# Kernel tuning notes

Hardware: AMD Instinct MI355X
Metric: run time of the kernel (lower is better)

## Reference

```python
import jax, jax.numpy as jnp
import numpy as np

HEADS = 56
OUT = 32       # hidden_channels (per-head out dim)
N_FEAT = 128
N_CLASS = 2
N_NODES = 20000
N_EDGES = 100000
N_GRAPHS = 50
EPS_BN = 1e-5


def _gat_conv(x, W, att_src, att_dst, bias, src, dst, n, concat):
    # x: [n, in]; W: [in, H*O]; att_*: [H, O]
    h = (x @ W).reshape(n, HEADS, OUT)                     # [n, H, O]
    a_s = jnp.sum(h * att_src, axis=-1)                    # [n, H]
    a_d = jnp.sum(h * att_dst, axis=-1)                    # [n, H]
    e = jax.nn.leaky_relu(a_s[src] + a_d[dst], 0.2)        # [E, H]
    m = jax.ops.segment_max(e, dst, num_segments=n)        # per-dst max
    ex = jnp.exp(e - m[dst])
    den = jax.ops.segment_sum(ex, dst, num_segments=n)
    alpha = ex / den[dst]                                  # segment softmax over incoming edges
    msg = h[src] * alpha[:, :, None]                       # [E, H, O]
    out = jax.ops.segment_sum(msg, dst, num_segments=n)    # [n, H, O]
    if concat:
        return out.reshape(n, HEADS * OUT) + bias
    return out.mean(axis=1) + bias


def _bn_eval(x, gamma, beta, mean, var):
    return (x - mean) * jax.lax.rsqrt(var + EPS_BN) * gamma + beta


def setup_inputs() -> dict:
    key = jax.random.key(0)
    ks = jax.random.split(key, 20)
    d1 = HEADS * OUT
    inp = {
        'x': jax.random.normal(ks[0], (N_NODES, N_FEAT), jnp.float32),
        'edge_index': jax.random.randint(ks[1], (2, N_EDGES), 0, N_NODES, jnp.int32),
        'batch': jnp.sort(jax.random.randint(ks[2], (N_NODES,), 0, N_GRAPHS, jnp.int32)),
        'W1': jax.random.normal(ks[3], (N_FEAT, d1), jnp.float32) * (1.0 / np.sqrt(N_FEAT)),
        'att_src1': jax.random.normal(ks[4], (HEADS, OUT), jnp.float32) * 0.1,
        'att_dst1': jax.random.normal(ks[5], (HEADS, OUT), jnp.float32) * 0.1,
        'b1': jnp.zeros((d1,), jnp.float32),
        'bn1_g': jnp.ones((d1,), jnp.float32),
        'bn1_b': jnp.zeros((d1,), jnp.float32),
        'bn1_m': jax.random.normal(ks[6], (d1,), jnp.float32) * 0.1,
        'bn1_v': jax.random.uniform(ks[7], (d1,), jnp.float32) + 0.5,
        'W2': jax.random.normal(ks[8], (d1, d1), jnp.float32) * (1.0 / np.sqrt(d1)),
        'att_src2': jax.random.normal(ks[9], (HEADS, OUT), jnp.float32) * 0.1,
        'att_dst2': jax.random.normal(ks[10], (HEADS, OUT), jnp.float32) * 0.1,
        'b2': jnp.zeros((OUT,), jnp.float32),
        'bn2_g': jnp.ones((OUT,), jnp.float32),
        'bn2_b': jnp.zeros((OUT,), jnp.float32),
        'bn2_m': jax.random.normal(ks[11], (OUT,), jnp.float32) * 0.1,
        'bn2_v': jax.random.uniform(ks[12], (OUT,), jnp.float32) + 0.5,
        'lin_w': jax.random.normal(ks[13], (OUT, N_CLASS), jnp.float32) * (1.0 / np.sqrt(OUT)),
        'lin_b': jnp.zeros((N_CLASS,), jnp.float32),
    }
    return inp


def reference(x, edge_index, batch, W1, att_src1, att_dst1, b1, bn1_g, bn1_b, bn1_m, bn1_v,
              W2, att_src2, att_dst2, b2, bn2_g, bn2_b, bn2_m, bn2_v, lin_w, lin_b):
    n = x.shape[0]
    loop = jnp.arange(n, dtype=edge_index.dtype)
    src = jnp.concatenate([edge_index[0], loop])   # PyG GATConv add_self_loops=True
    dst = jnp.concatenate([edge_index[1], loop])

    h = jax.nn.elu(_gat_conv(x, W1, att_src1, att_dst1, b1, src, dst, n, concat=True))
    h = _bn_eval(h, bn1_g, bn1_b, bn1_m, bn1_v)
    # dropout p=0.5 is identity in eval
    h = _gat_conv(h, W2, att_src2, att_dst2, b2, src, dst, n, concat=False)
    h = _bn_eval(h, bn2_g, bn2_b, bn2_m, bn2_v)

    sums = jax.ops.segment_sum(h, batch, num_segments=N_GRAPHS)
    cnt = jax.ops.segment_sum(jnp.ones((n, 1), h.dtype), batch, num_segments=N_GRAPHS)
    pooled = sums / jnp.maximum(cnt, 1.0)          # global_mean_pool
    return pooled @ lin_w + lin_b
```

## Files before the change

### kernel.cpp

```cpp
#include <hip/hip_runtime.h>
#include <hip/hip_bf16.h>
#include <hip/hip_fp8.h>
#include <cstdint>
#include <cstddef>

#define NN     20000
#define NF     128
#define NH     56
#define OC     32
#define DD1    1792
#define NE     100000
#define ETOT   120000
#define NG     50
#define EPS_BN 1e-5f
#define GRP    16
#define EB     16

typedef __bf16 bf16x8 __attribute__((ext_vector_type(8)));
typedef float  floatx4 __attribute__((ext_vector_type(4)));
typedef float  floatx2 __attribute__((ext_vector_type(2)));
typedef unsigned int u32;
typedef __attribute__((address_space(1))) u32 gu32;
typedef __attribute__((address_space(3))) u32 lu32;

__device__ __forceinline__ void async_copy16(void* lds, const void* g) {
    __builtin_amdgcn_global_load_lds((gu32*)const_cast<void*>(g), (lu32*)lds, 16, 0, 0);
}

__device__ __forceinline__ void dec_fp8x4(u32 u, float* v) {
#if __has_builtin(__builtin_amdgcn_cvt_pk_f32_fp8)
    floatx2 lo = __builtin_amdgcn_cvt_pk_f32_fp8(u, false);
    floatx2 hi = __builtin_amdgcn_cvt_pk_f32_fp8(u, true);
    v[0] = lo[0]; v[1] = lo[1]; v[2] = hi[0]; v[3] = hi[1];
#else
    #pragma unroll
    for (int b = 0; b < 4; ++b) {
        __hip_fp8_e4m3 t;
        t.__x = (u >> (8 * b)) & 0xff;
        v[b] = (float)t;
    }
#endif
}

__device__ __forceinline__ void fma_fp8x4(u32 u, float a, float* acc) {
    float v[4];
    dec_fp8x4(u, v);
    #pragma unroll
    for (int b = 0; b < 4; ++b) acc[b] += a * v[b];
}

__global__ __launch_bounds__(256) void cast_bf16_kernel(const float* __restrict__ in,
                                                        __hip_bfloat16* __restrict__ out, int n) {
    int i = blockIdx.x * 256 + threadIdx.x;
    if (i < n) out[i] = __float2bfloat16(in[i]);
}

__global__ __launch_bounds__(256) void transpose_cast_kernel(const float* __restrict__ in,
                                                             __hip_bfloat16* __restrict__ out,
                                                             int R, int C) {
    __shared__ float tile[32][33];
    int c0 = blockIdx.x * 32, r0 = blockIdx.y * 32;
    int tx = threadIdx.x & 31, ty = threadIdx.x >> 5;
    #pragma unroll
    for (int i = 0; i < 32; i += 8) {
        int r = r0 + ty + i, c = c0 + tx;
        if (r < R && c < C) tile[ty + i][tx] = in[(size_t)r * C + c];
    }
    __syncthreads();
    #pragma unroll
    for (int i = 0; i < 32; i += 8) {
        int c = c0 + ty + i, r = r0 + tx;
        if (c < C && r < R) out[(size_t)c * R + r] = __float2bfloat16(tile[tx][ty + i]);
    }
}

__global__ __launch_bounds__(256) void hist_kernel(const int* __restrict__ ei, int* __restrict__ deg) {
    int i = blockIdx.x * 256 + threadIdx.x;
    if (i >= ETOT) return;
    int dst = (i < NE) ? ei[NE + i] : (i - NE);
    atomicAdd(&deg[dst], 1);
}

__global__ __launch_bounds__(1024) void scan_kernel(const int* __restrict__ deg,
                                                    int* __restrict__ rowptr,
                                                    int* __restrict__ cursor) {
    __shared__ int buf[1024];
    int t = threadIdx.x;
    const int CH = (NN + 1023) >> 10;
    int base = t * CH;
    int s = 0;
    for (int j = 0; j < CH; ++j) { int idx = base + j; if (idx < NN) s += deg[idx]; }
    buf[t] = s;
    __syncthreads();
    for (int off = 1; off < 1024; off <<= 1) {
        int v = (t >= off) ? buf[t - off] : 0;
        __syncthreads();
        buf[t] += v;
        __syncthreads();
    }
    int run = buf[t] - s;
    for (int j = 0; j < CH; ++j) {
        int idx = base + j;
        if (idx < NN) { rowptr[idx] = run; cursor[idx] = run; run += deg[idx]; }
    }
    if (t == 1023) rowptr[NN] = buf[1023];
}

__global__ __launch_bounds__(256) void scatter_kernel(const int* __restrict__ ei,
                                                      int* __restrict__ cursor,
                                                      int* __restrict__ csr_src) {
    int i = blockIdx.x * 256 + threadIdx.x;
    if (i >= ETOT) return;
    int s, d;
    if (i < NE) { s = ei[i]; d = ei[NE + i]; } else { s = i - NE; d = i - NE; }
    int pos = atomicAdd(&cursor[d], 1);
    csr_src[pos] = s;
}

__global__ __launch_bounds__(512, 2) void gemm_192(const __hip_bfloat16* __restrict__ A,
                                                   const __hip_bfloat16* __restrict__ Bt,
                                                   unsigned char* __restrict__ C8,
                                                   int M, int N, int K) {
    __shared__ __align__(16) unsigned short lds[2][28672];
    const int tid  = threadIdx.x;
    const int lane = tid & 63, wave = tid >> 6;
    const int wm = wave >> 2, wn = wave & 3;

    const int nbx = N >> 8;
    const int nby = (M + 191) / 192;
    const int nwg = nbx * nby;
    const int q = nwg >> 3, r = nwg & 7;
    const int xcd = blockIdx.x & 7, bidx = blockIdx.x >> 3;
    const int wg = (xcd < r ? xcd * (q + 1) : r * (q + 1) + (xcd - r) * q) + bidx;
    const int by = wg / nbx, bx = wg - by * nbx;
    const int m0 = by * 192, n0 = bx << 8;

    const int NT = K >> 6;

    const int qq = lane >> 4, rr = lane & 15;

    auto stageA = [&](int kt, int b) {
        #pragma unroll
        for (int i = 0; i < 3; ++i) {
            int slot = i * 512 + tid;
            int row = slot >> 3, pch = slot & 7;
            int lc = pch ^ (row & 7);
            int gr = m0 + row; if (gr > M - 1) gr = M - 1;
            async_copy16(&lds[b][slot * 8], A + (size_t)gr * K + (kt << 6) + lc * 8);
        }
    };
    auto stageB = [&](int kt, int b) {
        #pragma unroll
        for (int i = 0; i < 4; ++i) {
            int slot = i * 512 + tid;
            int row = slot >> 3, pch = slot & 7;
            int lc = pch ^ (row & 7);
            async_copy16(&lds[b][12288 + slot * 8], Bt + (size_t)(n0 + row) * K + (kt << 6) + lc * 8);
        }
    };

    floatx4 zero = {0.f, 0.f, 0.f, 0.f};
    floatx4 acc[6][4];
    #pragma unroll
    for (int i = 0; i < 6; ++i)
        #pragma unroll
        for (int jj = 0; jj < 4; ++jj) acc[i][jj] = zero;

    bf16x8 aF[3][2], bA[2][2], bB[2][2];

    auto loadA = [&](int b, int mg) {
        #pragma unroll
        for (int mf = 0; mf < 3; ++mf)
            #pragma unroll
            for (int s = 0; s < 2; ++s) {
                int row = wm * 96 + mg * 48 + mf * 16 + rr;
                int pch = (s * 4 + qq) ^ (row & 7);
                aF[mf][s] = *(const bf16x8*)&lds[b][row * 64 + pch * 8];
            }
    };
    auto loadB = [&](int b, bf16x8 (&bF)[2][2], int ng) {
        #pragma unroll
        for (int nf = 0; nf < 2; ++nf)
            #pragma unroll
            for (int s = 0; s < 2; ++s) {
                int row = wn * 64 + (ng * 2 + nf) * 16 + rr;
                int pch = (s * 4 + qq) ^ (row & 7);
                bF[nf][s] = *(const bf16x8*)&lds[b][12288 + row * 64 + pch * 8];
            }
    };
    auto mfmaQ = [&](int mg, int ng, bf16x8 (&bF)[2][2]) {
        #pragma unroll
        for (int mf = 0; mf < 3; ++mf)
            #pragma unroll
            for (int nf = 0; nf < 2; ++nf)
                #pragma unroll
                for (int s = 0; s < 2; ++s)
                    acc[mg * 3 + mf][ng * 2 + nf] = __builtin_amdgcn_mfma_f32_16x16x32_bf16(
                        aF[mf][s], bF[nf][s], acc[mg * 3 + mf][ng * 2 + nf], 0, 0, 0);
    };

#define SB0 __builtin_amdgcn_sched_barrier(0)
#define GBAR do { SB0; __builtin_amdgcn_s_barrier(); SB0; } while (0)

    stageB(0, 0); stageA(0, 0);
    stageB(1, 1); stageA(1, 1);
    SB0;
    asm volatile("s_waitcnt vmcnt(7)" ::: "memory");
    GBAR;

    for (int t = 0; t < NT; ++t) {
        const int p = t & 1;
        int tp = t + 2; while (tp >= NT) tp -= 2;

        loadA(p, 0); loadB(p, bA, 0);
        GBAR;
        __builtin_amdgcn_s_setprio(1);
        mfmaQ(0, 0, bA);
        __builtin_amdgcn_s_setprio(0);
        GBAR;

        loadB(p, bB, 1);
        stageB(tp, p);
        GBAR;
        __builtin_amdgcn_s_setprio(1);
        mfmaQ(0, 1, bB);
        __builtin_amdgcn_s_setprio(0);
        GBAR;

        loadA(p, 1);
        stageA(tp, p);
        SB0;
        asm volatile("s_waitcnt vmcnt(7)" ::: "memory");
        GBAR;
        __builtin_amdgcn_s_setprio(1);
        mfmaQ(1, 1, bB);
        mfmaQ(1, 0, bA);
        __builtin_amdgcn_s_setprio(0);
        GBAR;
    }
#undef GBAR
#undef SB0

    #pragma unroll
    for (int mt = 0; mt < 6; ++mt) {
        #pragma unroll
        for (int r4 = 0; r4 < 4; ++r4) {
            int rowc = m0 + wm * 96 + mt * 16 + (lane >> 4) * 4 + r4;
            if (rowc < M) {
                float v0 = acc[mt][0][r4], v1 = acc[mt][1][r4];
                float v2 = acc[mt][2][r4], v3 = acc[mt][3][r4];
                unsigned char q8[4];
#if __has_builtin(__builtin_amdgcn_cvt_pk_fp8_f32)
                u32 p01 = (u32)__builtin_amdgcn_cvt_pk_fp8_f32(v0, v1, 0, false);
                u32 p23 = (u32)__builtin_amdgcn_cvt_pk_fp8_f32(v2, v3, 0, false);
                q8[0] = p01 & 0xff; q8[1] = (p01 >> 8) & 0xff;
                q8[2] = p23 & 0xff; q8[3] = (p23 >> 8) & 0xff;
#else
                { __hip_fp8_e4m3 t0(v0), t1(v1), t2(v2), t3(v3);
                  q8[0] = t0.__x; q8[1] = t1.__x; q8[2] = t2.__x; q8[3] = t3.__x; }
#endif
                #pragma unroll
                for (int nt = 0; nt < 4; ++nt) {
                    int col = n0 + wn * 64 + nt * 16 + (lane & 15);
                    C8[(size_t)rowc * N + col] = q8[nt];
                }
            }
        }
    }
}

__global__ __launch_bounds__(256) void attn_score(const unsigned char* __restrict__ h8,
                                                  const float* __restrict__ att_src,
                                                  const float* __restrict__ att_dst,
                                                  float* __restrict__ as_,
                                                  float* __restrict__ ad_) {
    int wave = threadIdx.x >> 6, lane = threadIdx.x & 63;
    int node = blockIdx.x * 4 + wave;
    if (node >= NN || lane >= NH) return;
    const uint2* hp = (const uint2*)(h8 + (size_t)node * DD1 + lane * OC);
    float s = 0.f, d = 0.f;
    #pragma unroll
    for (int jj = 0; jj < 4; ++jj) {
        uint2 u2 = hp[jj];
        u32 us[2] = {u2.x, u2.y};
        #pragma unroll
        for (int w = 0; w < 2; ++w) {
            float v[4];
            dec_fp8x4(us[w], v);
            #pragma unroll
            for (int b = 0; b < 4; ++b) {
                int o = jj * 8 + w * 4 + b;
                s += v[b] * att_src[lane * OC + o];
                d += v[b] * att_dst[lane * OC + o];
            }
        }
    }
    as_[(size_t)node * NH + lane] = s;
    ad_[(size_t)node * NH + lane] = d;
}

template <int LAYER>
__device__ __forceinline__ void flush_node(float* acc, float den, int cur, int f, int lane,
                                           const float* __restrict__ bias,
                                           const float* __restrict__ bng,
                                           const float* __restrict__ bnb,
                                           const float* __restrict__ bnm,
                                           const float* __restrict__ bnv,
                                           void* __restrict__ outp) {
    float inv = 1.f / den;
    #pragma unroll
    for (int k = 0; k < 4; ++k) acc[k] *= inv;

    if constexpr (LAYER == 1) {
        int d0 = f * 256 + lane * 4;
        u32 r01, r23;
        {
            float v0 = acc[0] + bias[d0 + 0];
            float v1 = acc[1] + bias[d0 + 1];
            float v2 = acc[2] + bias[d0 + 2];
            float v3 = acc[3] + bias[d0 + 3];
            v0 = v0 > 0.f ? v0 : expm1f(v0);
            v1 = v1 > 0.f ? v1 : expm1f(v1);
            v2 = v2 > 0.f ? v2 : expm1f(v2);
            v3 = v3 > 0.f ? v3 : expm1f(v3);
            v0 = (v0 - bnm[d0 + 0]) * rsqrtf(bnv[d0 + 0] + EPS_BN) * bng[d0 + 0] + bnb[d0 + 0];
            v1 = (v1 - bnm[d0 + 1]) * rsqrtf(bnv[d0 + 1] + EPS_BN) * bng[d0 + 1] + bnb[d0 + 1];
            v2 = (v2 - bnm[d0 + 2]) * rsqrtf(bnv[d0 + 2] + EPS_BN) * bng[d0 + 2] + bnb[d0 + 2];
            v3 = (v3 - bnm[d0 + 3]) * rsqrtf(bnv[d0 + 3] + EPS_BN) * bng[d0 + 3] + bnb[d0 + 3];
            __hip_bfloat16 b0 = __float2bfloat16(v0), b1 = __float2bfloat16(v1);
            __hip_bfloat16 b2 = __float2bfloat16(v2), b3 = __float2bfloat16(v3);
            r01 = (u32)*(unsigned short*)&b0 | ((u32)*(unsigned short*)&b1 << 16);
            r23 = (u32)*(unsigned short*)&b2 | ((u32)*(unsigned short*)&b3 << 16);
        }
        uint2 pk; pk.x = r01; pk.y = r23;
        *(uint2*)((__hip_bfloat16*)outp + (size_t)cur * DD1 + d0) = pk;
    } else {
        #pragma unroll
        for (int k = 0; k < 4; ++k) {
            acc[k] += __shfl_xor(acc[k], 8, 64);
            acc[k] += __shfl_xor(acc[k], 16, 64);
            acc[k] += __shfl_xor(acc[k], 32, 64);
        }
        if (lane < 8) {
            floatx4 pk;
            #pragma unroll
            for (int k = 0; k < 4; ++k) pk[k] = acc[k] * (1.f / NH);
            *(floatx4*)((float*)outp + ((size_t)cur * 7 + f) * OC + lane * 4) = pk;
        }
    }
    acc[0] = acc[1] = acc[2] = acc[3] = 0.f;
}

template <int LAYER>
__global__ __launch_bounds__(256) void attn_aggregate(const int* __restrict__ rowptr,
                                                      const int* __restrict__ csr_src,
                                                      const float* __restrict__ as_,
                                                      const float* __restrict__ ad_,
                                                      const unsigned char* __restrict__ h8,
                                                      const float* __restrict__ bias,
                                                      const float* __restrict__ bng,
                                                      const float* __restrict__ bnb,
                                                      const float* __restrict__ bnm,
                                                      const float* __restrict__ bnv,
                                                      void* __restrict__ outp) {
    const int wv = threadIdx.x >> 6, lane = threadIdx.x & 63;
    const int w = blockIdx.x * 4 + wv;
    const int NWAVES = 7 * (NN / GRP);
    if (w >= NWAVES) return;
    const int f  = w % 7;
    const int g  = w / 7;
    const int n0 = g * GRP;
    const int off  = f * 256 + lane * 4;
    const int head = f * 8 + (lane >> 3);

    const int e0 = rowptr[n0], e1 = rowptr[n0 + GRP];
    int cur = n0;
    int bound = rowptr[n0 + 1];
    float adv = ad_[(size_t)cur * NH + head];

    float acc[4] = {0.f, 0.f, 0.f, 0.f};
    float m = -1e30f, den = 0.f;

    for (int e = e0; e < e1; e += EB) {
        u32   hv[EB];
        float sv[EB];
        #pragma unroll
        for (int i = 0; i < EB; ++i) {
            int idx = (e + i < e1) ? e + i : e1 - 1;
            int s = csr_src[idx];
            hv[i] = *(const u32*)(h8 + (size_t)s * DD1 + off);
            sv[i] = as_[(size_t)s * NH + head];
        }
        #pragma unroll
        for (int i = 0; i < EB; ++i) {
            if (e + i >= e1) break;
            if (e + i >= bound) {
                flush_node<LAYER>(acc, den, cur, f, lane, bias, bng, bnb, bnm, bnv, outp);
                ++cur;
                bound = rowptr[cur + 1];
                adv = ad_[(size_t)cur * NH + head];
                m = -1e30f; den = 0.f;
            }
            float lr = sv[i] + adv;
            lr = lr > 0.f ? lr : 0.2f * lr;
            float wgt;
            if (lr > m) {
                float scale = __expf(m - lr);
                den = den * scale + 1.f;
                #pragma unroll
                for (int k = 0; k < 4; ++k) acc[k] *= scale;
                m = lr;
                wgt = 1.f;
            } else {
                wgt = __expf(lr - m);
                den += wgt;
            }
            fma_fp8x4(hv[i], wgt, acc);
        }
    }
    flush_node<LAYER>(acc, den, cur, f, lane, bias, bng, bnb, bnm, bnv, outp);
}

__global__ __launch_bounds__(256) void pool_kernel(const float* __restrict__ h2part,
                                                   const int* __restrict__ batch,
                                                   float* __restrict__ sums,
                                                   float* __restrict__ cnt) {
    __shared__ float red[4][OC];
    const int g = blockIdx.x >> 3, c = blockIdx.x & 7;
    const int t = threadIdx.x;
    const int ch = t & 31, nl = t >> 5;
    int lo = 0, hi = NN;
    while (lo < hi) { int mid = (lo + hi) >> 1; if (batch[mid] < g) lo = mid + 1; else hi = mid; }
    const int s = lo;
    hi = NN;
    while (lo < hi) { int mid = (lo + hi) >> 1; if (batch[mid] <= g) lo = mid + 1; else hi = mid; }
    const int e = lo;
    const int len = e - s;
    const int n0 = s + (len * c) / 8;
    const int n1 = s + (len * (c + 1)) / 8;
    float acc = 0.f;
    for (int n = n0 + nl; n < n1; n += 8) {
        const float* p = h2part + (size_t)n * 7 * OC + ch;
        float a = 0.f;
        #pragma unroll
        for (int f = 0; f < 7; ++f) a += p[f * OC];
        acc += a;
    }
    acc += __shfl_xor(acc, 32, 64);
    if ((t & 32) == 0) red[t >> 6][ch] = acc;
    __syncthreads();
    if (t < OC) {
        float total = red[0][t] + red[1][t] + red[2][t] + red[3][t];
        atomicAdd(&sums[g * OC + t], total);
    }
    if (t == 0 && c == 0) cnt[g] = (float)len;
}

__global__ __launch_bounds__(128) void final_kernel(const float* __restrict__ sums,
                                                    const float* __restrict__ cnt,
                                                    const float* __restrict__ b2,
                                                    const float* __restrict__ bn2g,
                                                    const float* __restrict__ bn2b,
                                                    const float* __restrict__ bn2m,
                                                    const float* __restrict__ bn2v,
                                                    const float* __restrict__ lin_w,
                                                    const float* __restrict__ lin_b,
                                                    float* __restrict__ out) {
    int t = threadIdx.x;
    if (t >= NG * 2) return;
    int g = t >> 1, c = t & 1;
    float invc = 1.f / fmaxf(cnt[g], 1.f);
    float acc = lin_b[c];
    #pragma unroll
    for (int o = 0; o < OC; ++o) {
        float pooled = sums[g * OC + o] * invc + b2[o];
        float v = (pooled - bn2m[o]) * rsqrtf(bn2v[o] + EPS_BN) * bn2g[o] + bn2b[o];
        acc += v * lin_w[o * 2 + c];
    }
    out[t] = acc;
}

extern "C" void kernel_launch(void* const* d_in, const int* in_sizes, int n_in,
                              void* d_out, int out_size, void* d_ws, size_t ws_size,
                              hipStream_t stream) {
    const float* x    = (const float*)d_in[0];
    const int*   ei   = (const int*)d_in[1];
    const int*   bat  = (const int*)d_in[2];
    const float* W1   = (const float*)d_in[3];
    const float* at_s1 = (const float*)d_in[4];
    const float* at_d1 = (const float*)d_in[5];
    const float* b1   = (const float*)d_in[6];
    const float* bn1g = (const float*)d_in[7];
    const float* bn1b = (const float*)d_in[8];
    const float* bn1m = (const float*)d_in[9];
    const float* bn1v = (const float*)d_in[10];
    const float* W2   = (const float*)d_in[11];
    const float* at_s2 = (const float*)d_in[12];
    const float* at_d2 = (const float*)d_in[13];
    const float* b2   = (const float*)d_in[14];
    const float* bn2g = (const float*)d_in[15];
    const float* bn2b = (const float*)d_in[16];
    const float* bn2m = (const float*)d_in[17];
    const float* bn2v = (const float*)d_in[18];
    const float* linw = (const float*)d_in[19];
    const float* linb = (const float*)d_in[20];
    float* out = (float*)d_out;

    char* wsp = (char*)d_ws;
    auto alloc = [&](size_t bytes) -> void* {
        void* p = (void*)wsp;
        wsp += (bytes + 255) & ~(size_t)255;
        return p;
    };
    unsigned char*  h8  = (unsigned char*)alloc((size_t)NN * DD1);
    __hip_bfloat16* h1p = (__hip_bfloat16*)alloc((size_t)NN * DD1 * 2);
    __hip_bfloat16* xb  = (__hip_bfloat16*)alloc((size_t)NN * NF * 2);
    __hip_bfloat16* w1t = (__hip_bfloat16*)alloc((size_t)DD1 * NF * 2);
    __hip_bfloat16* w2t = (__hip_bfloat16*)alloc((size_t)DD1 * DD1 * 2);
    float* asb   = (float*)alloc((size_t)NN * NH * 4);
    float* adb   = (float*)alloc((size_t)NN * NH * 4);
    int*   deg   = (int*)alloc((size_t)NN * 4);
    int*   rowp  = (int*)alloc((size_t)(NN + 1) * 4);
    int*   curs  = (int*)alloc((size_t)NN * 4);
    int*   csr   = (int*)alloc((size_t)ETOT * 4);
    float* h2part = (float*)alloc((size_t)NN * 7 * OC * 4);
    float* sums  = (float*)alloc((size_t)(NG * OC + NG) * 4);
    float* cnt   = sums + NG * OC;

    hipMemsetAsync(deg, 0, (size_t)NN * 4, stream);
    hipMemsetAsync(sums, 0, (size_t)(NG * OC + NG) * 4, stream);

    cast_bf16_kernel<<<(NN * NF + 255) / 256, 256, 0, stream>>>(x, xb, NN * NF);
    transpose_cast_kernel<<<dim3(DD1 / 32, NF / 32), 256, 0, stream>>>(W1, w1t, NF, DD1);
    transpose_cast_kernel<<<dim3(DD1 / 32, DD1 / 32), 256, 0, stream>>>(W2, w2t, DD1, DD1);
    hist_kernel<<<(ETOT + 255) / 256, 256, 0, stream>>>(ei, deg);
    scan_kernel<<<1, 1024, 0, stream>>>(deg, rowp, curs);
    scatter_kernel<<<(ETOT + 255) / 256, 256, 0, stream>>>(ei, curs, csr);

    const int AGG_BLOCKS = (7 * (NN / GRP) + 3) / 4;
    const int NBY192 = (NN + 191) / 192;
    const int GEMM_BLOCKS = NBY192 * (DD1 / 256);

    gemm_192<<<GEMM_BLOCKS, 512, 0, stream>>>(xb, w1t, h8, NN, DD1, NF);
    attn_score<<<NN / 4, 256, 0, stream>>>(h8, at_s1, at_d1, asb, adb);
    attn_aggregate<1><<<AGG_BLOCKS, 256, 0, stream>>>(rowp, csr, asb, adb, h8, b1, bn1g, bn1b, bn1m, bn1v, (void*)h1p);

    gemm_192<<<GEMM_BLOCKS, 512, 0, stream>>>(h1p, w2t, h8, NN, DD1, DD1);
    attn_score<<<NN / 4, 256, 0, stream>>>(h8, at_s2, at_d2, asb, adb);
    attn_aggregate<2><<<AGG_BLOCKS, 256, 0, stream>>>(rowp, csr, asb, adb, h8, b2, bn2g, bn2b, bn2m, bn2v, (void*)h2part);

    pool_kernel<<<NG * 8, 256, 0, stream>>>(h2part, bat, sums, cnt);
    final_kernel<<<1, 128, 0, stream>>>(sums, cnt, b2, bn2g, bn2b, bn2m, bn2v, linw, linb, out);
}
```

Before: 575.3 us.

## Precompute normalized attention coefficients in a separate per-edge kernel

Adds an attn_prep kernel that computes the leaky-relu logits, segment max and softmax denominator per destination node and writes normalized alpha per edge and head. The aggregate kernel then reads alpha directly and does a plain weighted sum, dropping the online-softmax rescaling and the redundant exp work across the 7 feature waves per head. In exchange it adds an extra kernel launch per layer and about 27 MB of alpha writes and reads per layer, plus a serial per-lane loop over edges in the prep kernel.

```diff
diff --git a/kernel.cpp b/kernel.cpp
--- a/kernel.cpp
+++ b/kernel.cpp
@@ -299,18 +299,40 @@
     ad_[(size_t)node * NH + lane] = d;
 }
 
+__global__ __launch_bounds__(256) void attn_prep(const int* __restrict__ rowptr,
+                                                 const int* __restrict__ csr_src,
+                                                 const float* __restrict__ as_,
+                                                 const float* __restrict__ ad_,
+                                                 float* __restrict__ alpha) {
+    int wv = threadIdx.x >> 6, lane = threadIdx.x & 63;
+    int n = blockIdx.x * 4 + wv;
+    if (n >= NN || lane >= NH) return;
+    float adv = ad_[(size_t)n * NH + lane];
+    int e0 = rowptr[n], e1 = rowptr[n + 1];
+    float m = -1e30f, den = 0.f;
+    for (int e = e0; e < e1; ++e) {
+        int s = csr_src[e];
+        float lr = as_[(size_t)s * NH + lane] + adv;
+        lr = lr > 0.f ? lr : 0.2f * lr;
+        alpha[(size_t)e * NH + lane] = lr;
+        if (lr > m) { den = den * __expf(m - lr) + 1.f; m = lr; }
+        else den += __expf(lr - m);
+    }
+    float inv = 1.f / den;
+    for (int e = e0; e < e1; ++e) {
+        float lr = alpha[(size_t)e * NH + lane];
+        alpha[(size_t)e * NH + lane] = __expf(lr - m) * inv;
+    }
+}
+
 template <int LAYER>
-__device__ __forceinline__ void flush_node(float* acc, float den, int cur, int f, int lane,
+__device__ __forceinline__ void flush_node(float* acc, int cur, int f, int lane,
                                            const float* __restrict__ bias,
                                            const float* __restrict__ bng,
                                            const float* __restrict__ bnb,
                                            const float* __restrict__ bnm,
                                            const float* __restrict__ bnv,
                                            void* __restrict__ outp) {
-    float inv = 1.f / den;
-    #pragma unroll
-    for (int k = 0; k < 4; ++k) acc[k] *= inv;
-
     if constexpr (LAYER == 1) {
         int d0 = f * 256 + lane * 4;
         u32 r01, r23;
@@ -354,8 +376,7 @@
 template <int LAYER>
 __global__ __launch_bounds__(256) void attn_aggregate(const int* __restrict__ rowptr,
                                                       const int* __restrict__ csr_src,
-                                                      const float* __restrict__ as_,
-                                                      const float* __restrict__ ad_,
+                                                      const float* __restrict__ alpha,
                                                       const unsigned char* __restrict__ h8,
                                                       const float* __restrict__ bias,
                                                       const float* __restrict__ bng,
@@ -376,49 +397,31 @@
     const int e0 = rowptr[n0], e1 = rowptr[n0 + GRP];
     int cur = n0;
     int bound = rowptr[n0 + 1];
-    float adv = ad_[(size_t)cur * NH + head];
 
     float acc[4] = {0.f, 0.f, 0.f, 0.f};
-    float m = -1e30f, den = 0.f;
 
     for (int e = e0; e < e1; e += EB) {
         u32   hv[EB];
-        float sv[EB];
+        float av[EB];
         #pragma unroll
         for (int i = 0; i < EB; ++i) {
             int idx = (e + i < e1) ? e + i : e1 - 1;
+            av[i] = alpha[(size_t)idx * NH + head];
             int s = csr_src[idx];
             hv[i] = *(const u32*)(h8 + (size_t)s * DD1 + off);
-            sv[i] = as_[(size_t)s * NH + head];
         }
         #pragma unroll
         for (int i = 0; i < EB; ++i) {
             if (e + i >= e1) break;
             if (e + i >= bound) {
-                flush_node<LAYER>(acc, den, cur, f, lane, bias, bng, bnb, bnm, bnv, outp);
+                flush_node<LAYER>(acc, cur, f, lane, bias, bng, bnb, bnm, bnv, outp);
                 ++cur;
                 bound = rowptr[cur + 1];
-                adv = ad_[(size_t)cur * NH + head];
-                m = -1e30f; den = 0.f;
             }
-            float lr = sv[i] + adv;
-            lr = lr > 0.f ? lr : 0.2f * lr;
-            float wgt;
-            if (lr > m) {
-                float scale = __expf(m - lr);
-                den = den * scale + 1.f;
-                #pragma unroll
-                for (int k = 0; k < 4; ++k) acc[k] *= scale;
-                m = lr;
-                wgt = 1.f;
-            } else {
-                wgt = __expf(lr - m);
-                den += wgt;
-            }
-            fma_fp8x4(hv[i], wgt, acc);
-        }
-    }
-    flush_node<LAYER>(acc, den, cur, f, lane, bias, bng, bnb, bnm, bnv, outp);
+            fma_fp8x4(hv[i], av[i], acc);
+        }
+    }
+    flush_node<LAYER>(acc, cur, f, lane, bias, bng, bnb, bnm, bnv, outp);
 }
 
 __global__ __launch_bounds__(256) void pool_kernel(const float* __restrict__ h2part,
@@ -519,6 +522,7 @@
     __hip_bfloat16* w2t = (__hip_bfloat16*)alloc((size_t)DD1 * DD1 * 2);
     float* asb   = (float*)alloc((size_t)NN * NH * 4);
     float* adb   = (float*)alloc((size_t)NN * NH * 4);
+    float* alpha = (float*)alloc((size_t)ETOT * NH * 4);
     int*   deg   = (int*)alloc((size_t)NN * 4);
     int*   rowp  = (int*)alloc((size_t)(NN + 1) * 4);
     int*   curs  = (int*)alloc((size_t)NN * 4);
@@ -543,11 +547,13 @@
 
     gemm_192<<<GEMM_BLOCKS, 512, 0, stream>>>(xb, w1t, h8, NN, DD1, NF);
     attn_score<<<NN / 4, 256, 0, stream>>>(h8, at_s1, at_d1, asb, adb);
-    attn_aggregate<1><<<AGG_BLOCKS, 256, 0, stream>>>(rowp, csr, asb, adb, h8, b1, bn1g, bn1b, bn1m, bn1v, (void*)h1p);
+    attn_prep<<<NN / 4, 256, 0, stream>>>(rowp, csr, asb, adb, alpha);
+    attn_aggregate<1><<<AGG_BLOCKS, 256, 0, stream>>>(rowp, csr, alpha, h8, b1, bn1g, bn1b, bn1m, bn1v, (void*)h1p);
 
     gemm_192<<<GEMM_BLOCKS, 512, 0, stream>>>(h1p, w2t, h8, NN, DD1, DD1);
     attn_score<<<NN / 4, 256, 0, stream>>>(h8, at_s2, at_d2, asb, adb);
-    attn_aggregate<2><<<AGG_BLOCKS, 256, 0, stream>>>(rowp, csr, asb, adb, h8, b2, bn2g, bn2b, bn2m, bn2v, (void*)h2part);
+    attn_prep<<<NN / 4, 256, 0, stream>>>(rowp, csr, asb, adb, alpha);
+    attn_aggregate<2><<<AGG_BLOCKS, 256, 0, stream>>>(rowp, csr, alpha, h8, b2, bn2g, bn2b, bn2m, bn2v, (void*)h2part);
 
     pool_kernel<<<NG * 8, 256, 0, stream>>>(h2part, bat, sums, cnt);
     final_kernel<<<1, 128, 0, stream>>>(sums, cnt, b2, bn2g, bn2b, bn2m, bn2v, linw, linb, out);
```

New measurement: 591.3 us. 1.03x slower.

## Use 4-wave GEMM blocks with larger per-wave output tiles

Applied to the files above, without the earlier changes.

Reorganizes the 192x256 GEMM tile from 8 waves (2x4, 96x64 per wave) to 4 waves (2x2, 96x128 per wave). Each wave now holds twice as many accumulators and B fragments, and the MFMA phases are split into four quadrants with an extra barrier. Staging loops double their iterations and the vmcnt wait is adjusted to match. The aim is more register-level reuse of A fragments and less LDS traffic per MFMA, at the cost of heavier register pressure, one block per CU, and fewer waves to hide latency.

```diff
diff --git a/kernel.cpp b/kernel.cpp
--- a/kernel.cpp
+++ b/kernel.cpp
@@ -117,14 +117,14 @@
     csr_src[pos] = s;
 }
 
-__global__ __launch_bounds__(512, 2) void gemm_192(const __hip_bfloat16* __restrict__ A,
+__global__ __launch_bounds__(256, 1) void gemm_192(const __hip_bfloat16* __restrict__ A,
                                                    const __hip_bfloat16* __restrict__ Bt,
                                                    unsigned char* __restrict__ C8,
                                                    int M, int N, int K) {
     __shared__ __align__(16) unsigned short lds[2][28672];
     const int tid  = threadIdx.x;
     const int lane = tid & 63, wave = tid >> 6;
-    const int wm = wave >> 2, wn = wave & 3;
+    const int wm = wave >> 1, wn = wave & 1;
 
     const int nbx = N >> 8;
     const int nby = (M + 191) / 192;
@@ -141,8 +141,8 @@
 
     auto stageA = [&](int kt, int b) {
         #pragma unroll
-        for (int i = 0; i < 3; ++i) {
-            int slot = i * 512 + tid;
+        for (int i = 0; i < 6; ++i) {
+            int slot = i * 256 + tid;
             int row = slot >> 3, pch = slot & 7;
             int lc = pch ^ (row & 7);
             int gr = m0 + row; if (gr > M - 1) gr = M - 1;
@@ -151,8 +151,8 @@
     };
     auto stageB = [&](int kt, int b) {
         #pragma unroll
-        for (int i = 0; i < 4; ++i) {
-            int slot = i * 512 + tid;
+        for (int i = 0; i < 8; ++i) {
+            int slot = i * 256 + tid;
             int row = slot >> 3, pch = slot & 7;
             int lc = pch ^ (row & 7);
             async_copy16(&lds[b][12288 + slot * 8], Bt + (size_t)(n0 + row) * K + (kt << 6) + lc * 8);
@@ -160,13 +160,13 @@
     };
 
     floatx4 zero = {0.f, 0.f, 0.f, 0.f};
-    floatx4 acc[6][4];
+    floatx4 acc[6][8];
     #pragma unroll
     for (int i = 0; i < 6; ++i)
         #pragma unroll
-        for (int jj = 0; jj < 4; ++jj) acc[i][jj] = zero;
-
-    bf16x8 aF[3][2], bA[2][2], bB[2][2];
+        for (int jj = 0; jj < 8; ++jj) acc[i][jj] = zero;
+
+    bf16x8 aF[3][2], bF0[4][2], bF1[4][2];
 
     auto loadA = [&](int b, int mg) {
         #pragma unroll
@@ -178,25 +178,25 @@
                 aF[mf][s] = *(const bf16x8*)&lds[b][row * 64 + pch * 8];
             }
     };
-    auto loadB = [&](int b, bf16x8 (&bF)[2][2], int ng) {
-        #pragma unroll
-        for (int nf = 0; nf < 2; ++nf)
+    auto loadB = [&](int b, bf16x8 (&bF)[4][2], int ng) {
+        #pragma unroll
+        for (int nf = 0; nf < 4; ++nf)
             #pragma unroll
             for (int s = 0; s < 2; ++s) {
-                int row = wn * 64 + (ng * 2 + nf) * 16 + rr;
+                int row = wn * 128 + (ng * 4 + nf) * 16 + rr;
                 int pch = (s * 4 + qq) ^ (row & 7);
                 bF[nf][s] = *(const bf16x8*)&lds[b][12288 + row * 64 + pch * 8];
             }
     };
-    auto mfmaQ = [&](int mg, int ng, bf16x8 (&bF)[2][2]) {
+    auto mfmaQ = [&](int mg, int ng, bf16x8 (&bF)[4][2]) {
         #pragma unroll
         for (int mf = 0; mf < 3; ++mf)
             #pragma unroll
-            for (int nf = 0; nf < 2; ++nf)
+            for (int nf = 0; nf < 4; ++nf)
                 #pragma unroll
                 for (int s = 0; s < 2; ++s)
-                    acc[mg * 3 + mf][ng * 2 + nf] = __builtin_amdgcn_mfma_f32_16x16x32_bf16(
-                        aF[mf][s], bF[nf][s], acc[mg * 3 + mf][ng * 2 + nf], 0, 0, 0);
+                    acc[mg * 3 + mf][ng * 4 + nf] = __builtin_amdgcn_mfma_f32_16x16x32_bf16(
+                        aF[mf][s], bF[nf][s], acc[mg * 3 + mf][ng * 4 + nf], 0, 0, 0);
     };
 
 #define SB0 __builtin_amdgcn_sched_barrier(0)
@@ -205,36 +205,41 @@
     stageB(0, 0); stageA(0, 0);
     stageB(1, 1); stageA(1, 1);
     SB0;
-    asm volatile("s_waitcnt vmcnt(7)" ::: "memory");
+    asm volatile("s_waitcnt vmcnt(14)" ::: "memory");
     GBAR;
 
     for (int t = 0; t < NT; ++t) {
         const int p = t & 1;
         int tp = t + 2; while (tp >= NT) tp -= 2;
 
-        loadA(p, 0); loadB(p, bA, 0);
+        loadA(p, 0); loadB(p, bF0, 0);
         GBAR;
         __builtin_amdgcn_s_setprio(1);
-        mfmaQ(0, 0, bA);
+        mfmaQ(0, 0, bF0);
         __builtin_amdgcn_s_setprio(0);
         GBAR;
 
-        loadB(p, bB, 1);
+        loadB(p, bF1, 1);
         stageB(tp, p);
         GBAR;
         __builtin_amdgcn_s_setprio(1);
-        mfmaQ(0, 1, bB);
+        mfmaQ(0, 1, bF1);
         __builtin_amdgcn_s_setprio(0);
         GBAR;
 
         loadA(p, 1);
         stageA(tp, p);
+        GBAR;
+        __builtin_amdgcn_s_setprio(1);
+        mfmaQ(1, 1, bF1);
+        __builtin_amdgcn_s_setprio(0);
+        GBAR;
+
         SB0;
-        asm volatile("s_waitcnt vmcnt(7)" ::: "memory");
+        asm volatile("s_waitcnt vmcnt(14)" ::: "memory");
         GBAR;
         __builtin_amdgcn_s_setprio(1);
-        mfmaQ(1, 1, bB);
-        mfmaQ(1, 0, bA);
+        mfmaQ(1, 0, bF0);
         __builtin_amdgcn_s_setprio(0);
         GBAR;
     }
@@ -247,21 +252,21 @@
         for (int r4 = 0; r4 < 4; ++r4) {
             int rowc = m0 + wm * 96 + mt * 16 + (lane >> 4) * 4 + r4;
             if (rowc < M) {
-                float v0 = acc[mt][0][r4], v1 = acc[mt][1][r4];
-                float v2 = acc[mt][2][r4], v3 = acc[mt][3][r4];
-                unsigned char q8[4];
+                unsigned char q8[8];
+                #pragma unroll
+                for (int pr = 0; pr < 4; ++pr) {
+                    float v0 = acc[mt][2 * pr][r4], v1 = acc[mt][2 * pr + 1][r4];
 #if __has_builtin(__builtin_amdgcn_cvt_pk_fp8_f32)
-                u32 p01 = (u32)__builtin_amdgcn_cvt_pk_fp8_f32(v0, v1, 0, false);
-                u32 p23 = (u32)__builtin_amdgcn_cvt_pk_fp8_f32(v2, v3, 0, false);
-                q8[0] = p01 & 0xff; q8[1] = (p01 >> 8) & 0xff;
-                q8[2] = p23 & 0xff; q8[3] = (p23 >> 8) & 0xff;
+                    u32 pk = (u32)__builtin_amdgcn_cvt_pk_fp8_f32(v0, v1, 0, false);
+                    q8[2 * pr] = pk & 0xff; q8[2 * pr + 1] = (pk >> 8) & 0xff;
 #else
-                { __hip_fp8_e4m3 t0(v0), t1(v1), t2(v2), t3(v3);
-                  q8[0] = t0.__x; q8[1] = t1.__x; q8[2] = t2.__x; q8[3] = t3.__x; }
+                    { __hip_fp8_e4m3 t0(v0), t1(v1);
+                      q8[2 * pr] = t0.__x; q8[2 * pr + 1] = t1.__x; }
 #endif
+                }
                 #pragma unroll
-                for (int nt = 0; nt < 4; ++nt) {
-                    int col = n0 + wn * 64 + nt * 16 + (lane & 15);
+                for (int nt = 0; nt < 8; ++nt) {
+                    int col = n0 + wn * 128 + nt * 16 + (lane & 15);
                     C8[(size_t)rowc * N + col] = q8[nt];
                 }
             }
@@ -541,11 +546,11 @@
     const int NBY192 = (NN + 191) / 192;
     const int GEMM_BLOCKS = NBY192 * (DD1 / 256);
 
-    gemm_192<<<GEMM_BLOCKS, 512, 0, stream>>>(xb, w1t, h8, NN, DD1, NF);
+    gemm_192<<<GEMM_BLOCKS, 256, 0, stream>>>(xb, w1t, h8, NN, DD1, NF);
     attn_score<<<NN / 4, 256, 0, stream>>>(h8, at_s1, at_d1, asb, adb);
     attn_aggregate<1><<<AGG_BLOCKS, 256, 0, stream>>>(rowp, csr, asb, adb, h8, b1, bn1g, bn1b, bn1m, bn1v, (void*)h1p);
 
-    gemm_192<<<GEMM_BLOCKS, 512, 0, stream>>>(h1p, w2t, h8, NN, DD1, DD1);
+    gemm_192<<<GEMM_BLOCKS, 256, 0, stream>>>(h1p, w2t, h8, NN, DD1, DD1);
     attn_score<<<NN / 4, 256, 0, stream>>>(h8, at_s2, at_d2, asb, adb);
     attn_aggregate<2><<<AGG_BLOCKS, 256, 0, stream>>>(rowp, csr, asb, adb, h8, b2, bn2g, bn2b, bn2m, bn2v, (void*)h2part);
 
```

Result: slower. 602.0 us (+4.6%).

## Store fp8 features as per-slice planes and double-buffer edge gathers in aggregation

Applied to the files above, without the earlier changes.

The fp8 GEMM output is stored as seven column-slice planes of 256 bytes per node instead of row-major 1792-byte rows. Each aggregation wave then gathers from a compact plane, and waves are mapped slice-major so concurrently running waves touch the same plane, which should improve L2 locality. The edge gather loop is also software-pipelined with two register buffers so loads for the next batch overlap the softmax/FMA work of the current batch. The cost is more register pressure, and the prefetch may read a batch past the end, which is clamped to the last valid index.

```diff
diff --git a/kernel.cpp b/kernel.cpp
--- a/kernel.cpp
+++ b/kernel.cpp
@@ -15,6 +15,7 @@
 #define EPS_BN 1e-5f
 #define GRP    16
 #define EB     16
+#define NGROUPS (NN / GRP)
 
 typedef __bf16 bf16x8 __attribute__((ext_vector_type(8)));
 typedef float  floatx4 __attribute__((ext_vector_type(4)));
@@ -261,8 +262,8 @@
 #endif
                 #pragma unroll
                 for (int nt = 0; nt < 4; ++nt) {
-                    int col = n0 + wn * 64 + nt * 16 + (lane & 15);
-                    C8[(size_t)rowc * N + col] = q8[nt];
+                    int inner = wn * 64 + nt * 16 + (lane & 15);
+                    C8[(size_t)bx * NN * 256 + (size_t)rowc * 256 + inner] = q8[nt];
                 }
             }
         }
@@ -277,7 +278,8 @@
     int wave = threadIdx.x >> 6, lane = threadIdx.x & 63;
     int node = blockIdx.x * 4 + wave;
     if (node >= NN || lane >= NH) return;
-    const uint2* hp = (const uint2*)(h8 + (size_t)node * DD1 + lane * OC);
+    const uint2* hp = (const uint2*)(h8 + (size_t)(lane >> 3) * NN * 256
+                                        + (size_t)node * 256 + (lane & 7) * OC);
     float s = 0.f, d = 0.f;
     #pragma unroll
     for (int jj = 0; jj < 4; ++jj) {
@@ -365,12 +367,13 @@
                                                       void* __restrict__ outp) {
     const int wv = threadIdx.x >> 6, lane = threadIdx.x & 63;
     const int w = blockIdx.x * 4 + wv;
-    const int NWAVES = 7 * (NN / GRP);
+    const int NWAVES = 7 * NGROUPS;
     if (w >= NWAVES) return;
-    const int f  = w % 7;
-    const int g  = w / 7;
+    const int f = w / NGROUPS;
+    const int g = w - f * NGROUPS;
     const int n0 = g * GRP;
-    const int off  = f * 256 + lane * 4;
+    const unsigned char* hslice = h8 + (size_t)f * NN * 256;
+    const int loff = lane * 4;
     const int head = f * 8 + (lane >> 3);
 
     const int e0 = rowptr[n0], e1 = rowptr[n0 + GRP];
@@ -381,20 +384,23 @@
     float acc[4] = {0.f, 0.f, 0.f, 0.f};
     float m = -1e30f, den = 0.f;
 
-    for (int e = e0; e < e1; e += EB) {
-        u32   hv[EB];
-        float sv[EB];
+    u32 hvA[EB], hvB[EB];
+    float svA[EB], svB[EB];
+
+    auto loadBatch = [&](int eb, u32* hv, float* sv) {
         #pragma unroll
         for (int i = 0; i < EB; ++i) {
-            int idx = (e + i < e1) ? e + i : e1 - 1;
+            int idx = eb + i; if (idx > e1 - 1) idx = e1 - 1;
             int s = csr_src[idx];
-            hv[i] = *(const u32*)(h8 + (size_t)s * DD1 + off);
+            hv[i] = *(const u32*)(hslice + (size_t)s * 256 + loff);
             sv[i] = as_[(size_t)s * NH + head];
         }
+    };
+    auto computeBatch = [&](int eb, u32* hv, float* sv) {
         #pragma unroll
         for (int i = 0; i < EB; ++i) {
-            if (e + i >= e1) break;
-            if (e + i >= bound) {
+            if (eb + i >= e1) break;
+            if (eb + i >= bound) {
                 flush_node<LAYER>(acc, den, cur, f, lane, bias, bng, bnb, bnm, bnv, outp);
                 ++cur;
                 bound = rowptr[cur + 1];
@@ -417,6 +423,14 @@
             }
             fma_fp8x4(hv[i], wgt, acc);
         }
+    };
+
+    loadBatch(e0, hvA, svA);
+    for (int e = e0; e < e1; e += 2 * EB) {
+        loadBatch(e + EB, hvB, svB);
+        computeBatch(e, hvA, svA);
+        loadBatch(e + 2 * EB, hvA, svA);
+        computeBatch(e + EB, hvB, svB);
     }
     flush_node<LAYER>(acc, den, cur, f, lane, bias, bng, bnb, bnm, bnv, outp);
 }
@@ -537,7 +551,7 @@
     scan_kernel<<<1, 1024, 0, stream>>>(deg, rowp, curs);
     scatter_kernel<<<(ETOT + 255) / 256, 256, 0, stream>>>(ei, curs, csr);
 
-    const int AGG_BLOCKS = (7 * (NN / GRP) + 3) / 4;
+    const int AGG_BLOCKS = (7 * NGROUPS + 3) / 4;
     const int NBY192 = (NN + 191) / 192;
     const int GEMM_BLOCKS = NBY192 * (DD1 / 256);
 
```

Result: slower. 635.0 us (+10.4%).
